# Kernel tuning notes

Hardware: AMD Instinct MI355X
Metric: run time of the kernel (lower is better)

Reference implementation:

```python
import jax, jax.numpy as jnp
import numpy as np

B, C_IN, T, H, W = 4, 256, 8, 56, 56
C_OUT = 256
KT, KH, KW = 1, 3, 3
PH, PW = 1, 1
SH, SW = 1, 1


def setup_inputs() -> dict:
    key = jax.random.key(0)
    k1, k2, k3, k4 = jax.random.split(key, 4)
    x = jax.random.normal(k1, (B, C_IN, T, H, W), dtype=jnp.float32)
    alpha = jax.random.normal(k2, (B, C_IN, T, 1, 1), dtype=jnp.float32)
    # base weight: torch shape (1,1,c_out,c_in//g,kt,kh,kw); store squeezed
    fan_in = C_IN * KT * KH * KW
    bound_w = float(np.sqrt(6.0 / fan_in))  # kaiming_uniform a=sqrt(5) -> U(-sqrt(6/fan_in), +)
    weight = jax.random.uniform(k3, (C_OUT, C_IN, KT, KH, KW), dtype=jnp.float32,
                                minval=-bound_w, maxval=bound_w)
    bound_b = float(1.0 / np.sqrt(fan_in))
    bias = jax.random.uniform(k4, (C_OUT,), dtype=jnp.float32, minval=-bound_b, maxval=bound_b)
    return {"x": x, "alpha": alpha, "weight": weight, "bias": bias}


def reference(x, alpha, weight, bias):
    b, c_in, t, h, w = x.shape
    c_out, _, kt, kh, kw = weight.shape
    pad_t = kt // 2
    # temporal unfold: pad t by kt//2 on both sides, gather kt-wide windows
    xp = jnp.pad(x, ((0, 0), (0, 0), (pad_t, pad_t), (0, 0), (0, 0)))
    idx = jnp.arange(t)[:, None] + jnp.arange(kt)[None, :]  # (t, kt)
    xu = xp[:, :, idx]                                      # (b, c_in, t, kt, h, w)
    xu = jnp.transpose(xu, (0, 2, 1, 3, 4, 5)).reshape(b * t, c_in, kt, h, w)
    # per-frame weights: W_t = alpha_t * W_base  (cal_dim='cin' -> alpha scales c_in axis)
    a = jnp.transpose(alpha[..., 0, 0], (0, 2, 1))          # (b, t, c_in)
    wts = a[:, :, None, :, None, None, None] * weight[None, None]  # (b, t, c_out, c_in, kt, kh, kw)
    wts = wts.reshape(b * t, c_out, c_in, kt, kh, kw)

    def conv_one(xi, wi):
        # xi: (c_in, kt, h, w), wi: (c_out, c_in, kt, kh, kw)
        o = jax.lax.conv_general_dilated(
            xi[None], wi,
            window_strides=(1, SH, SW),
            padding=((0, 0), (PH, PH), (PW, PW)),
            dimension_numbers=('NCDHW', 'OIDHW', 'NCDHW'))
        return o[0, :, 0]  # (c_out, h_out, w_out); depth collapses to 1

    out = jax.vmap(conv_one)(xu, wts)                       # (b*t, c_out, h_out, w_out)
    out = out + bias[None, :, None, None]
    h_out, w_out = out.shape[-2], out.shape[-1]
    out = out.reshape(b, t, c_out, h_out, w_out).transpose(0, 2, 1, 3, 4)
    return out
```

## Files before the change

### kernel.cpp

```cpp
#include <hip/hip_runtime.h>
#include <hip/hip_bf16.h>

typedef __attribute__((ext_vector_type(8))) short short8;
typedef __attribute__((ext_vector_type(4))) float floatx4;

#define C_INN 256
#define T_N   8
#define H_N   56
#define W_N   56
#define C_OUTN 256
#define HW_N  (H_N * W_N)
#define THW   (T_N * HW_N)
#define NTAP  9
#define LDX_S 40

#define GLOAD_LDS16(gp, lp) \
  __builtin_amdgcn_global_load_lds((const __attribute__((address_space(1))) void*)(gp), \
                                   (__attribute__((address_space(3))) void*)(lp), 16, 0, 0)

__global__ void prep_weight(const float* __restrict__ w, __hip_bfloat16* __restrict__ wb) {
    int idx = blockIdx.x * blockDim.x + threadIdx.x;
    if (idx >= C_OUTN * NTAP * C_INN) return;
    int e    = idx & 7;
    int c    = (idx >> 3) % 2304;
    int g4   = (idx >> 3) / 2304;
    int r    = c & 63;
    int tq   = c >> 6;
    int quad = tq & 3, tap = tq >> 2;
    int cg = g4 >> 2, mtile = g4 & 3;
    int o  = mtile * 64 + r;
    int ci = cg * 32 + quad * 8 + e;
    wb[idx] = __float2bfloat16(w[(o * C_INN + ci) * NTAP + tap]);
}

__global__ __launch_bounds__(256, 2) void tada_conv(
    const float* __restrict__ x, const float* __restrict__ alpha,
    const __hip_bfloat16* __restrict__ wb, const float* __restrict__ bias,
    float* __restrict__ out)
{
    __shared__ __hip_bfloat16 lA[2304 * 8];
    __shared__ __hip_bfloat16 lX[340 * LDX_S];

    const int tid   = threadIdx.x;
    const int mtile = blockIdx.x;
    const int ntile = blockIdx.y;
    const int bt    = blockIdx.z;
    const int b = bt >> 3, t = bt & 7;
    const int h0 = (ntile % 7) * 8;
    const int w0 = (ntile / 7) * 32;

    const int wn   = tid >> 6;
    const int lane = tid & 63;
    const int col = lane & 15, quad = lane >> 4;

    const int cil = tid >> 5;
    const int pxl = tid & 31;

    int xoff[11];
#pragma unroll
    for (int it = 0; it < 11; ++it) {
        int px = pxl + it * 32;
        int hi = px / 34;
        int wi = px - hi * 34;
        int hh = h0 - 1 + hi;
        int ww = w0 - 1 + wi;
        bool inimg = (px < 340) && ((unsigned)hh < (unsigned)H_N) && ((unsigned)ww < (unsigned)W_N);
        xoff[it] = inimg ? (hh * W_N + ww) : -1;
    }

    floatx4 acc[4][4];
#pragma unroll
    for (int i = 0; i < 4; ++i)
#pragma unroll
        for (int j = 0; j < 4; ++j)
            acc[i][j] = (floatx4){0.f, 0.f, 0.f, 0.f};

    const long xbase = ((long)b * C_INN) * THW + (long)t * HW_N;
    const int  abase = b * C_INN * T_N + t;

    floatx4 pX[11];
    float   pa0, pa1, pa2, pa3;

    auto PREFETCH = [&](int cgp) {
        const int ci0 = cgp * 32 + cil * 4;
        pa0 = alpha[abase + (ci0 + 0) * T_N];
        pa1 = alpha[abase + (ci0 + 1) * T_N];
        pa2 = alpha[abase + (ci0 + 2) * T_N];
        pa3 = alpha[abase + (ci0 + 3) * T_N];
        const float* xc = x + xbase + (long)ci0 * THW;
#pragma unroll
        for (int it = 0; it < 11; ++it) {
            float v0 = 0.f, v1 = 0.f, v2 = 0.f, v3 = 0.f;
            if (xoff[it] >= 0) {
                const float* xp = xc + xoff[it];
                v0 = xp[0];
                v1 = xp[THW];
                v2 = xp[2 * THW];
                v3 = xp[3 * THW];
            }
            pX[it] = (floatx4){v0, v1, v2, v3};
        }
    };

    PREFETCH(0);

    for (int cg = 0; cg < 8; ++cg) {
        __syncthreads();

        {
            const __hip_bfloat16* wsrc = wb + ((long)(cg * 4 + mtile) * 2304) * 8;
            const int cb = wn * 64;
#pragma unroll
            for (int it = 0; it < 9; ++it) {
                GLOAD_LDS16(wsrc + (long)(it * 256 + cb + lane) * 8,
                            (char*)lA + (it * 256 + cb) * 16);
            }
        }

#pragma unroll
        for (int it = 0; it < 11; ++it) {
            int px = pxl + it * 32;
            if (it < 10 || pxl < 20) {
                union { __hip_bfloat16 h[4]; unsigned long long u; } pk;
                pk.h[0] = __float2bfloat16(pX[it][0] * pa0);
                pk.h[1] = __float2bfloat16(pX[it][1] * pa1);
                pk.h[2] = __float2bfloat16(pX[it][2] * pa2);
                pk.h[3] = __float2bfloat16(pX[it][3] * pa3);
                *reinterpret_cast<unsigned long long*>(&lX[px * LDX_S + cil * 4]) = pk.u;
            }
        }

        __syncthreads();

        if (cg < 7) PREFETCH(cg + 1);

        const __hip_bfloat16* lAr = lA + quad * 512 + col * 8;
#pragma unroll
        for (int kh = 0; kh < 3; ++kh) {
#pragma unroll
            for (int kw = 0; kw < 3; ++kw) {
                const int tap = kh * 3 + kw;
                short8 af[4], bf[4];
#pragma unroll
                for (int mi = 0; mi < 4; ++mi)
                    af[mi] = *(const short8*)(lAr + tap * 2048 + mi * 128);
#pragma unroll
                for (int ni = 0; ni < 4; ++ni) {
                    int g  = wn * 4 + ni;
                    int px = ((g >> 1) + kh) * 34 + (g & 1) * 16 + col + kw;
                    bf[ni] = *(const short8*)(lX + px * LDX_S + quad * 8);
                }
#pragma unroll
                for (int mi = 0; mi < 4; ++mi)
#pragma unroll
                    for (int ni = 0; ni < 4; ++ni)
                        acc[mi][ni] = __builtin_amdgcn_mfma_f32_16x16x32_bf16(
                            af[mi], bf[ni], acc[mi][ni], 0, 0, 0);
            }
        }
    }

#pragma unroll
    for (int mi = 0; mi < 4; ++mi) {
        const floatx4 bv = *(const floatx4*)(bias + mtile * 64 + mi * 16 + quad * 4);
#pragma unroll
        for (int ni = 0; ni < 4; ++ni) {
            int n  = wn * 64 + ni * 16 + col;
            int ph = n >> 5, pw = n & 31;
            if (w0 + pw < W_N) {
#pragma unroll
                for (int r = 0; r < 4; ++r) {
                    int m = mtile * 64 + mi * 16 + quad * 4 + r;
                    out[(((long)b * C_OUTN + m) * T_N + t) * HW_N + (h0 + ph) * W_N + (w0 + pw)]
                        = acc[mi][ni][r] + bv[r];
                }
            }
        }
    }
}

extern "C" void kernel_launch(void* const* d_in, const int* in_sizes, int n_in,
                              void* d_out, int out_size, void* d_ws, size_t ws_size,
                              hipStream_t stream) {
    const float* x      = (const float*)d_in[0];
    const float* alpha  = (const float*)d_in[1];
    const float* weight = (const float*)d_in[2];
    const float* bias   = (const float*)d_in[3];
    float* out = (float*)d_out;

    __hip_bfloat16* wb = (__hip_bfloat16*)d_ws;

    int nprep = C_OUTN * NTAP * C_INN;
    prep_weight<<<(nprep + 255) / 256, 256, 0, stream>>>(weight, wb);

    dim3 grid(4, 14, 32);
    tada_conv<<<grid, 256, 0, stream>>>(x, alpha, wb, bias, out);
}
```

Measured before the change: 338.5 us.

## Remap block order for XCD locality and widen per-thread channel staging

Grid flattened to 1D with a swizzle: consecutive block ids are spread across the 8 XCDs, so the four mtiles sharing one x tile end up on the same XCD and its L2. The x staging now has each thread load 8 channels for 6 pixel slots instead of 4 channels for 11, writing 16-byte LDS stores instead of 8-byte ones. The aim is better L2 reuse of x and weights, plus fewer, wider LDS writes. In exchange it uses more registers per thread and makes the global loads less coalesced, since 4 lanes now share a pixel and consecutive lanes stride by channel.

```diff
diff --git a/kernel.cpp b/kernel.cpp
--- a/kernel.cpp
+++ b/kernel.cpp
@@ -41,10 +41,13 @@
     __shared__ __hip_bfloat16 lA[2304 * 8];
     __shared__ __hip_bfloat16 lX[340 * LDX_S];
 
-    const int tid   = threadIdx.x;
-    const int mtile = blockIdx.x;
-    const int ntile = blockIdx.y;
-    const int bt    = blockIdx.z;
+    const int tid = threadIdx.x;
+
+    const int id  = blockIdx.x;
+    const int nid = (id & 7) * 224 + (id >> 3);
+    const int mtile = nid & 3;
+    const int ntile = (nid >> 2) % 14;
+    const int bt    = nid / 56;
     const int b = bt >> 3, t = bt & 7;
     const int h0 = (ntile % 7) * 8;
     const int w0 = (ntile / 7) * 32;
@@ -53,13 +56,13 @@
     const int lane = tid & 63;
     const int col = lane & 15, quad = lane >> 4;
 
-    const int cil = tid >> 5;
-    const int pxl = tid & 31;
+    const int cil4 = tid & 3;
+    const int pxl  = tid >> 2;
 
-    int xoff[11];
+    int xoff[6];
 #pragma unroll
-    for (int it = 0; it < 11; ++it) {
-        int px = pxl + it * 32;
+    for (int it = 0; it < 6; ++it) {
+        int px = pxl + it * 64;
         int hi = px / 34;
         int wi = px - hi * 34;
         int hh = h0 - 1 + hi;
@@ -78,27 +81,27 @@
     const long xbase = ((long)b * C_INN) * THW + (long)t * HW_N;
     const int  abase = b * C_INN * T_N + t;
 
-    floatx4 pX[11];
-    float   pa0, pa1, pa2, pa3;
+    float pX[6][8];
+    float pa[8];
 
     auto PREFETCH = [&](int cgp) {
-        const int ci0 = cgp * 32 + cil * 4;
-        pa0 = alpha[abase + (ci0 + 0) * T_N];
-        pa1 = alpha[abase + (ci0 + 1) * T_N];
-        pa2 = alpha[abase + (ci0 + 2) * T_N];
-        pa3 = alpha[abase + (ci0 + 3) * T_N];
+        const int ci0 = cgp * 32 + cil4 * 8;
+#pragma unroll
+        for (int j = 0; j < 8; ++j)
+            pa[j] = alpha[abase + (ci0 + j) * T_N];
         const float* xc = x + xbase + (long)ci0 * THW;
 #pragma unroll
-        for (int it = 0; it < 11; ++it) {
-            float v0 = 0.f, v1 = 0.f, v2 = 0.f, v3 = 0.f;
+        for (int it = 0; it < 6; ++it) {
             if (xoff[it] >= 0) {
                 const float* xp = xc + xoff[it];
-                v0 = xp[0];
-                v1 = xp[THW];
-                v2 = xp[2 * THW];
-                v3 = xp[3 * THW];
+#pragma unroll
+                for (int j = 0; j < 8; ++j)
+                    pX[it][j] = xp[j * THW];
+            } else {
+#pragma unroll
+                for (int j = 0; j < 8; ++j)
+                    pX[it][j] = 0.f;
             }
-            pX[it] = (floatx4){v0, v1, v2, v3};
         }
     };
 
@@ -118,15 +121,14 @@
         }
 
 #pragma unroll
-        for (int it = 0; it < 11; ++it) {
-            int px = pxl + it * 32;
-            if (it < 10 || pxl < 20) {
-                union { __hip_bfloat16 h[4]; unsigned long long u; } pk;
-                pk.h[0] = __float2bfloat16(pX[it][0] * pa0);
-                pk.h[1] = __float2bfloat16(pX[it][1] * pa1);
-                pk.h[2] = __float2bfloat16(pX[it][2] * pa2);
-                pk.h[3] = __float2bfloat16(pX[it][3] * pa3);
-                *reinterpret_cast<unsigned long long*>(&lX[px * LDX_S + cil * 4]) = pk.u;
+        for (int it = 0; it < 6; ++it) {
+            int px = pxl + it * 64;
+            if (it < 5 || pxl < 20) {
+                union { __hip_bfloat16 h[8]; short8 v; } pk;
+#pragma unroll
+                for (int j = 0; j < 8; ++j)
+                    pk.h[j] = __float2bfloat16(pX[it][j] * pa[j]);
+                *reinterpret_cast<short8*>(&lX[px * LDX_S + cil4 * 8]) = pk.v;
             }
         }
 
@@ -193,6 +195,5 @@
     int nprep = C_OUTN * NTAP * C_INN;
     prep_weight<<<(nprep + 255) / 256, 256, 0, stream>>>(weight, wb);
 
-    dim3 grid(4, 14, 32);
-    tada_conv<<<grid, 256, 0, stream>>>(x, alpha, wb, bias, out);
+    tada_conv<<<dim3(1792), 256, 0, stream>>>(x, alpha, wb, bias, out);
 }
```

New measurement: 358.7 us. +6.0%, slower.
